# Performance work log

Measured on AMD Instinct MI355X. Metric: run time of the kernel, lower is better.

## Reference

```python
import jax, jax.numpy as jnp
import numpy as np

N = 100000      # total nodes
E = 800000      # directed edges
DIN = 256       # input feature dim
H = 128         # hidden dim
EPS = 1e-5      # BatchNorm eps


def setup_inputs() -> dict:
    key = jax.random.key(0)
    ks = jax.random.split(key, 18)
    s = 0.05
    return {
        "x": jax.random.normal(ks[0], (N, DIN), jnp.float32),
        "src": jax.random.randint(ks[1], (E,), 0, N, dtype=jnp.int32),
        "dst": jax.random.randint(ks[2], (E,), 0, N, dtype=jnp.int32),
        "W1": jax.random.normal(ks[3], (DIN, H), jnp.float32) * s,
        "b1": jnp.zeros((H,), jnp.float32),
        "g1": jnp.ones((H,), jnp.float32),
        "be1": jnp.zeros((H,), jnp.float32),
        "W2": jax.random.normal(ks[4], (H, H), jnp.float32) * s,
        "b2": jnp.zeros((H,), jnp.float32),
        "g2": jnp.ones((H,), jnp.float32),
        "be2": jnp.zeros((H,), jnp.float32),
        "W3": jax.random.normal(ks[5], (H, H), jnp.float32) * s,
        "b3": jnp.zeros((H,), jnp.float32),
        "g3": jnp.ones((H,), jnp.float32),
        "be3": jnp.zeros((H,), jnp.float32),
        "Wf": jax.random.normal(ks[6], (H, 1), jnp.float32) * s,
        "bf": jnp.zeros((1,), jnp.float32),
    }


def _gcn_conv(h, W, b, src, dst, dis):
    # GCNConv: project, then sym-normalized aggregation over edges + self-loops
    h = h @ W                                   # [N, out]
    coef = dis[src] * dis[dst]                  # [E] edge norm weights
    agg = jax.ops.segment_sum(h[src] * coef[:, None], dst, num_segments=N)
    agg = agg + h * (dis * dis)[:, None]        # self-loop term (norm = 1/deg)
    return agg + b


def _bn_relu(h, g, be):
    # BatchNorm1d in training mode (batch stats over nodes, biased variance)
    mu = jnp.mean(h, axis=0)
    var = jnp.var(h, axis=0)
    return jax.nn.relu((h - mu) * (g / jnp.sqrt(var + EPS)) + be)


def reference(x, src, dst, W1, b1, g1, be1, W2, b2, g2, be2,
              W3, b3, g3, be3, Wf, bf):
    # degree of (A + I) counted on destination nodes, edge weight 1
    deg = jax.ops.segment_sum(jnp.ones((E,), jnp.float32), dst, num_segments=N) + 1.0
    dis = jax.lax.rsqrt(deg)                    # deg >= 1, safe

    h = _bn_relu(_gcn_conv(x, W1, b1, src, dst, dis), g1, be1)
    h = _bn_relu(_gcn_conv(h, W2, b2, src, dst, dis), g2, be2)
    h = _bn_relu(_gcn_conv(h, W3, b3, src, dst, dis), g3, be3)
    return h @ Wf + bf                          # [N, 1]
```

## Files before the change

### kernel.cpp

```cpp
#include <hip/hip_runtime.h>
#include <hip/hip_bf16.h>

typedef unsigned short ushort_t;
typedef __bf16 bf16x8 __attribute__((ext_vector_type(8)));
typedef unsigned short ushort8 __attribute__((ext_vector_type(8)));
typedef float f32x4 __attribute__((ext_vector_type(4)));

#define HH 128
#define EPS 1e-5f
#define STAT_SLICES 32

__device__ __forceinline__ float bf2f(ushort_t u) {
    unsigned v = ((unsigned)u) << 16;
    return __builtin_bit_cast(float, v);
}
__device__ __forceinline__ ushort_t f2bf(float f) {
    unsigned u = __builtin_bit_cast(unsigned, f);
    unsigned r = (u + 0x7fffu + ((u >> 16) & 1u)) >> 16;
    return (ushort_t)r;
}
__device__ __forceinline__ float cvt(const void* p, int i, int flag) {
    return flag ? bf2f(((const ushort_t*)p)[i]) : ((const float*)p)[i];
}

__global__ void setupK(const void* g1, const void* b1, const void* b2, const void* b3,
                       const void* g2, const void* g3,
                       const void* be1, const void* be2, const void* be3,
                       const void* Wf, const void* bfp,
                       float* __restrict__ cvec, int* __restrict__ flagp) {
    __shared__ int sflag;
    int t = threadIdx.x;
    if (t == 0) {
        int f = (((const ushort_t*)g1)[0] == 0x3F80) ? 1 : 0;
        sflag = f;
        flagp[0] = f;
    }
    __syncthreads();
    int f = sflag;
    cvec[t]         = cvt(b1, t, f);
    cvec[128 + t]   = cvt(b2, t, f);
    cvec[256 + t]   = cvt(b3, t, f);
    cvec[384 + t]   = cvt(g1, t, f);
    cvec[512 + t]   = cvt(g2, t, f);
    cvec[640 + t]   = cvt(g3, t, f);
    cvec[768 + t]   = cvt(be1, t, f);
    cvec[896 + t]   = cvt(be2, t, f);
    cvec[1024 + t]  = cvt(be3, t, f);
    cvec[1152 + t]  = cvt(Wf, t, f);
    if (t == 0) cvec[1280] = cvt(bfp, 0, f);
}

__global__ void histK(const int* __restrict__ dst, int* __restrict__ counts, int E) {
    int e = blockIdx.x * 256 + threadIdx.x;
    if (e < E) atomicAdd(&counts[dst[e]], 1);
}

__global__ void disK(const int* __restrict__ counts, float* __restrict__ dis, int n) {
    int i = blockIdx.x * 256 + threadIdx.x;
    if (i < n) dis[i] = rsqrtf((float)counts[i] + 1.0f);
}

__global__ void scanA(const int* __restrict__ cnt, int* __restrict__ partial, int n) {
    __shared__ int lds[256];
    int tid = threadIdx.x;
    int base = blockIdx.x * 2048 + tid * 8;
    int s = 0;
#pragma unroll
    for (int j = 0; j < 8; ++j) { int idx = base + j; if (idx < n) s += cnt[idx]; }
    lds[tid] = s; __syncthreads();
    for (int off = 128; off; off >>= 1) { if (tid < off) lds[tid] += lds[tid + off]; __syncthreads(); }
    if (tid == 0) partial[blockIdx.x] = lds[0];
}

__global__ void scanB(int* __restrict__ partial, int* __restrict__ rowptr, int nb, int n) {
    if (threadIdx.x == 0) {
        int running = 0;
        for (int i = 0; i < nb; ++i) { int v = partial[i]; partial[i] = running; running += v; }
        rowptr[n] = running;
    }
}

__global__ void scanC(const int* __restrict__ cnt, const int* __restrict__ partial,
                      int* __restrict__ rowptr, int n) {
    __shared__ int lds[256];
    int tid = threadIdx.x;
    int base = blockIdx.x * 2048 + tid * 8;
    int v[8]; int s = 0;
#pragma unroll
    for (int j = 0; j < 8; ++j) { int idx = base + j; v[j] = (idx < n) ? cnt[idx] : 0; s += v[j]; }
    lds[tid] = s; __syncthreads();
    for (int off = 1; off < 256; off <<= 1) {
        int x = (tid >= off) ? lds[tid - off] : 0;
        __syncthreads();
        lds[tid] += x;
        __syncthreads();
    }
    int excl = lds[tid] - s;
    int off0 = partial[blockIdx.x] + excl;
#pragma unroll
    for (int j = 0; j < 8; ++j) {
        int idx = base + j;
        if (idx < n) { rowptr[idx] = off0; off0 += v[j]; }
    }
}

__global__ void scatterK(const int* __restrict__ src, const int* __restrict__ dst,
                         const int* __restrict__ rowptr, int* __restrict__ fill,
                         const float* __restrict__ dis,
                         uint2* __restrict__ erec, int E) {
    int e = blockIdx.x * 256 + threadIdx.x;
    if (e >= E) return;
    int d = dst[e], s = src[e];
    int old = atomicSub(&fill[d], 1);
    int pos = rowptr[d] + old - 1;
    float c = dis[s] * dis[d];
    uint2 r; r.x = (unsigned)s; r.y = __builtin_bit_cast(unsigned, c);
    erec[pos] = r;
}

__global__ void trK(const void* __restrict__ W1, ushort_t* __restrict__ Wt1,
                    const void* __restrict__ W2, ushort_t* __restrict__ Wt2,
                    const void* __restrict__ W3, ushort_t* __restrict__ Wt3,
                    const int* __restrict__ flagp) {
    int idx = blockIdx.x * 256 + threadIdx.x;
    int flag = flagp[0];
    const void* W; ushort_t* Wt; int Kp;
    if (idx < 32768)       { W = W1; Wt = Wt1; Kp = 264; }
    else if (idx < 49152)  { W = W2; Wt = Wt2; Kp = 136; idx -= 32768; }
    else if (idx < 65536)  { W = W3; Wt = Wt3; Kp = 136; idx -= 49152; }
    else return;
    int k = idx >> 7, n = idx & 127;
    ushort_t v = flag ? ((const ushort_t*)W)[idx] : f2bf(((const float*)W)[idx]);
    Wt[n * Kp + k] = v;
}

template <bool BN, bool EXT, int K>
__global__ __launch_bounds__(256) void mmK(const void* __restrict__ Av,
                                           const ushort_t* __restrict__ Wt,
                                           ushort_t* __restrict__ out,
                                           int n,
                                           const float* __restrict__ scale,
                                           const float* __restrict__ shift,
                                           const int* __restrict__ flagp) {
    constexpr int KP  = K + 8;
    constexpr int BKP = 136;
    constexpr int NCH = K / 128;
    constexpr int NST = K / 32;

    __shared__ ushort_t bs[128 * BKP];

    const int tid  = threadIdx.x;
    const int lane = tid & 63;
    const int wave = tid >> 6;
    const int m = lane & 15;
    const int q = lane >> 4;
    const int flag = EXT ? flagp[0] : 1;

    int rowA = blockIdx.x * 64 + wave * 16 + m;
    int rA = rowA < n ? rowA : (n - 1);

    ushort8 a[NST];
    if (EXT && !flag) {
        const float* ap32 = (const float*)Av + (size_t)rA * K + q * 8;
#pragma unroll
        for (int s = 0; s < NST; ++s) {
            float4 f0 = *(const float4*)(ap32 + s * 32);
            float4 f1 = *(const float4*)(ap32 + s * 32 + 4);
            a[s][0] = f2bf(f0.x); a[s][1] = f2bf(f0.y); a[s][2] = f2bf(f0.z); a[s][3] = f2bf(f0.w);
            a[s][4] = f2bf(f1.x); a[s][5] = f2bf(f1.y); a[s][6] = f2bf(f1.z); a[s][7] = f2bf(f1.w);
        }
    } else {
        const ushort_t* ap16 = (const ushort_t*)Av + (size_t)rA * K + q * 8;
#pragma unroll
        for (int s = 0; s < NST; ++s) a[s] = *(const ushort8*)(ap16 + s * 32);
    }
    if (BN) {
#pragma unroll
        for (int s = 0; s < NST; ++s) {
            int kb = s * 32 + q * 8;
#pragma unroll
            for (int j = 0; j < 8; ++j) {
                float f = fmaxf(bf2f(a[s][j]) * scale[kb + j] + shift[kb + j], 0.f);
                a[s][j] = f2bf(f);
            }
        }
    }

    f32x4 acc[8];
#pragma unroll
    for (int t = 0; t < 8; ++t) acc[t] = (f32x4){0.f, 0.f, 0.f, 0.f};

#pragma unroll
    for (int c = 0; c < NCH; ++c) {
#pragma unroll
        for (int r = 0; r < 8; ++r) {
            int idx = tid + r * 256;
            int row = idx >> 4, seg = idx & 15;
            *(uint4*)&bs[row * BKP + seg * 8] =
                *(const uint4*)&Wt[(size_t)row * KP + c * 128 + seg * 8];
        }
        __syncthreads();
#pragma unroll
        for (int s = 0; s < 4; ++s) {
            bf16x8 af = __builtin_bit_cast(bf16x8, a[c * 4 + s]);
#pragma unroll
            for (int t = 0; t < 8; ++t) {
                ushort8 bv = *(const ushort8*)&bs[(t * 16 + m) * BKP + s * 32 + q * 8];
                acc[t] = __builtin_amdgcn_mfma_f32_16x16x32_bf16(
                    af, __builtin_bit_cast(bf16x8, bv), acc[t], 0, 0, 0);
            }
        }
        if (c + 1 < NCH) __syncthreads();
    }

    const int rb = blockIdx.x * 64 + wave * 16 + q * 4;
#pragma unroll
    for (int t = 0; t < 8; ++t) {
#pragma unroll
        for (int r = 0; r < 4; ++r) {
            int rr = rb + r;
            if (rr < n) out[(size_t)rr * HH + t * 16 + m] = f2bf(acc[t][r]);
        }
    }
}

__global__ __launch_bounds__(256) void aggK(const ushort_t* __restrict__ t,
                                            const uint2* __restrict__ erec,
                                            const int* __restrict__ rowptr,
                                            const float* __restrict__ dis,
                                            const float* __restrict__ bias,
                                            ushort_t* __restrict__ g,
                                            float* __restrict__ ssum, float* __restrict__ ssq,
                                            int n) {
    const int lane = threadIdx.x & 63;
    const int wave = threadIdx.x >> 6;
    const int cb = lane * 2;
    const float b0 = bias[cb], b1 = bias[cb + 1];
    float s0 = 0.f, s1 = 0.f, q0 = 0.f, q1 = 0.f;

    for (int node = blockIdx.x * 4 + wave; node < n; node += gridDim.x * 4) {
        float d = dis[node];
        float d2 = d * d;
        unsigned sv = *(const unsigned*)(t + (size_t)node * HH + cb);
        float a0 = bf2f((ushort_t)(sv & 0xffff)) * d2;
        float a1 = bf2f((ushort_t)(sv >> 16)) * d2;

        int beg = rowptr[node], end = rowptr[node + 1];
        for (int eb = beg; eb < end; eb += 64) {
            int rem = end - eb; if (rem > 64) rem = 64;
            uint2 rec = (lane < rem) ? erec[eb + lane] : (uint2){0u, 0u};
            int es = (int)rec.x;
            float ec = __builtin_bit_cast(float, rec.y);
            int rr = (rem + 7) & ~7;
            for (int j = 0; j < rr; j += 8) {
                int   ii[8]; float cc[8]; unsigned ww[8];
#pragma unroll
                for (int k = 0; k < 8; ++k) {
                    ii[k] = __shfl(es, j + k);
                    cc[k] = __shfl(ec, j + k);
                }
#pragma unroll
                for (int k = 0; k < 8; ++k)
                    ww[k] = *(const unsigned*)(t + (size_t)ii[k] * HH + cb);
#pragma unroll
                for (int k = 0; k < 8; ++k) {
                    a0 += bf2f((ushort_t)(ww[k] & 0xffff)) * cc[k];
                    a1 += bf2f((ushort_t)(ww[k] >> 16)) * cc[k];
                }
            }
        }
        a0 += b0; a1 += b1;
        unsigned packed = (unsigned)f2bf(a0) | ((unsigned)f2bf(a1) << 16);
        *(unsigned*)(g + (size_t)node * HH + cb) = packed;
        s0 += a0; s1 += a1; q0 += a0 * a0; q1 += a1 * a1;
    }

    __shared__ float red[4][64][4];
    red[wave][lane][0] = s0; red[wave][lane][1] = s1;
    red[wave][lane][2] = q0; red[wave][lane][3] = q1;
    __syncthreads();
    if (wave == 0) {
        float S0 = 0, S1 = 0, Q0 = 0, Q1 = 0;
#pragma unroll
        for (int w = 0; w < 4; ++w) {
            S0 += red[w][lane][0]; S1 += red[w][lane][1];
            Q0 += red[w][lane][2]; Q1 += red[w][lane][3];
        }
        int slice = (blockIdx.x & (STAT_SLICES - 1)) * HH;
        atomicAdd(&ssum[slice + cb], S0);
        atomicAdd(&ssum[slice + cb + 1], S1);
        atomicAdd(&ssq[slice + cb], Q0);
        atomicAdd(&ssq[slice + cb + 1], Q1);
    }
}

__global__ void finK(const float* __restrict__ ssum, const float* __restrict__ ssq,
                     const float* __restrict__ gam, const float* __restrict__ bet,
                     float* __restrict__ scale, float* __restrict__ shift, int n) {
    int c = threadIdx.x;
    float S = 0.f, Q = 0.f;
    for (int sl = 0; sl < STAT_SLICES; ++sl) { S += ssum[sl * HH + c]; Q += ssq[sl * HH + c]; }
    float invn = 1.0f / (float)n;
    float mu = S * invn;
    float var = Q * invn - mu * mu;
    var = fmaxf(var, 0.f);
    float sc = gam[c] * rsqrtf(var + EPS);
    scale[c] = sc;
    shift[c] = bet[c] - mu * sc;
}

__global__ __launch_bounds__(256) void outK(const ushort_t* __restrict__ g,
                                            const float* __restrict__ scale,
                                            const float* __restrict__ shift,
                                            const float* __restrict__ Wf,
                                            const float* __restrict__ bfp,
                                            void* __restrict__ outv, int n,
                                            const int* __restrict__ flagp) {
    const int lane = threadIdx.x & 63;
    const int wave = threadIdx.x >> 6;
    const int cb = lane * 2;
    const float w0 = Wf[cb], w1 = Wf[cb + 1];
    const float sc0 = scale[cb], sc1 = scale[cb + 1];
    const float sh0 = shift[cb], sh1 = shift[cb + 1];
    const float bb = bfp[0];
    const int flag = flagp[0];

    for (int node = blockIdx.x * 4 + wave; node < n; node += gridDim.x * 4) {
        unsigned v = *(const unsigned*)(g + (size_t)node * HH + cb);
        float h0 = fmaxf(bf2f((ushort_t)(v & 0xffff)) * sc0 + sh0, 0.f);
        float h1 = fmaxf(bf2f((ushort_t)(v >> 16)) * sc1 + sh1, 0.f);
        float x = h0 * w0 + h1 * w1;
#pragma unroll
        for (int off = 32; off; off >>= 1) x += __shfl_down(x, off);
        if (lane == 0) {
            float r = x + bb;
            if (flag) ((ushort_t*)outv)[node] = f2bf(r);
            else      ((float*)outv)[node] = r;
        }
    }
}

extern "C" void kernel_launch(void* const* d_in, const int* in_sizes, int n_in,
                              void* d_out, int out_size, void* d_ws, size_t ws_size,
                              hipStream_t stream) {
    const int DIN = 256;
    const int N = in_sizes[0] / DIN;
    const int E = in_sizes[1];

    const void* x   = d_in[0];
    const int*  src = (const int*)d_in[1];
    const int*  dst = (const int*)d_in[2];
    const void* W1  = d_in[3];
    const void* b1  = d_in[4];
    const void* g1  = d_in[5];
    const void* be1 = d_in[6];
    const void* W2  = d_in[7];
    const void* b2  = d_in[8];
    const void* g2  = d_in[9];
    const void* be2 = d_in[10];
    const void* W3  = d_in[11];
    const void* b3  = d_in[12];
    const void* g3  = d_in[13];
    const void* be3 = d_in[14];
    const void* Wf  = d_in[15];
    const void* bfp = d_in[16];

    char* base = (char*)d_ws;
    size_t off = 0;
    auto carve = [&](size_t bytes) -> void* {
        void* p = base + off;
        off += (bytes + 255) & ~(size_t)255;
        return p;
    };
    int*      counts = (int*)carve((size_t)N * 4);
    float*    stats  = (float*)carve((size_t)3 * 2 * STAT_SLICES * HH * 4);
    size_t    zbytes = off;
    float*    dis    = (float*)carve((size_t)N * 4);
    int*      rowptr = (int*)carve((size_t)(N + 1) * 4);
    int*      partial= (int*)carve(256 * 4);
    uint2*    erec   = (uint2*)carve((size_t)E * 8);
    ushort_t* Wt1    = (ushort_t*)carve((size_t)128 * 264 * 2);
    ushort_t* Wt2    = (ushort_t*)carve((size_t)128 * 136 * 2);
    ushort_t* Wt3    = (ushort_t*)carve((size_t)128 * 136 * 2);
    ushort_t* tbuf   = (ushort_t*)carve((size_t)N * HH * 2);
    ushort_t* gbuf   = (ushort_t*)carve((size_t)N * HH * 2);
    float*    cvec   = (float*)carve((size_t)1281 * 4);
    int*      flagp  = (int*)carve(256);

    float* ssum0 = stats;                         float* ssq0 = ssum0 + STAT_SLICES * HH;
    float* ssum1 = ssq0 + STAT_SLICES * HH;       float* ssq1 = ssum1 + STAT_SLICES * HH;
    float* ssum2 = ssq1 + STAT_SLICES * HH;       float* ssq2 = ssum2 + STAT_SLICES * HH;

    float* scsh = cvec + 1344;
    float* scshbuf = (float*)carve((size_t)3 * 2 * HH * 4);
    float* scale0 = scshbuf;         float* shift0 = scale0 + HH;
    float* scale1 = shift0 + HH;     float* shift1 = scale1 + HH;
    float* scale2 = shift1 + HH;     float* shift2 = scale2 + HH;
    (void)scsh;

    float* c_b1 = cvec;         float* c_b2 = cvec + 128;  float* c_b3 = cvec + 256;
    float* c_g1 = cvec + 384;   float* c_g2 = cvec + 512;  float* c_g3 = cvec + 640;
    float* c_be1 = cvec + 768;  float* c_be2 = cvec + 896; float* c_be3 = cvec + 1024;
    float* c_Wf = cvec + 1152;  float* c_bf = cvec + 1280;

    const int nb = (N + 2047) / 2048;

    hipMemsetAsync(d_ws, 0, zbytes, stream);

    setupK<<<1, 128, 0, stream>>>(g1, b1, b2, b3, g2, g3, be1, be2, be3, Wf, bfp, cvec, flagp);

    histK<<<(E + 255) / 256, 256, 0, stream>>>(dst, counts, E);
    disK<<<(N + 255) / 256, 256, 0, stream>>>(counts, dis, N);
    scanA<<<nb, 256, 0, stream>>>(counts, partial, N);
    scanB<<<1, 64, 0, stream>>>(partial, rowptr, nb, N);
    scanC<<<nb, 256, 0, stream>>>(counts, partial, rowptr, N);
    scatterK<<<(E + 255) / 256, 256, 0, stream>>>(src, dst, rowptr, counts, dis, erec, E);

    trK<<<256, 256, 0, stream>>>(W1, Wt1, W2, Wt2, W3, Wt3, flagp);

    const int mmBlocks = (N + 63) / 64;
    const int aggBlocks = 4096;

    mmK<false, true, 256><<<mmBlocks, 256, 0, stream>>>(x, Wt1, tbuf, N, nullptr, nullptr, flagp);
    aggK<<<aggBlocks, 256, 0, stream>>>(tbuf, erec, rowptr, dis, c_b1, gbuf, ssum0, ssq0, N);
    finK<<<1, 128, 0, stream>>>(ssum0, ssq0, c_g1, c_be1, scale0, shift0, N);
    mmK<true, false, 128><<<mmBlocks, 256, 0, stream>>>(gbuf, Wt2, tbuf, N, scale0, shift0, flagp);
    aggK<<<aggBlocks, 256, 0, stream>>>(tbuf, erec, rowptr, dis, c_b2, gbuf, ssum1, ssq1, N);
    finK<<<1, 128, 0, stream>>>(ssum1, ssq1, c_g2, c_be2, scale1, shift1, N);
    mmK<true, false, 128><<<mmBlocks, 256, 0, stream>>>(gbuf, Wt3, tbuf, N, scale1, shift1, flagp);
    aggK<<<aggBlocks, 256, 0, stream>>>(tbuf, erec, rowptr, dis, c_b3, gbuf, ssum2, ssq2, N);
    finK<<<1, 128, 0, stream>>>(ssum2, ssq2, c_g3, c_be3, scale2, shift2, N);
    outK<<<1024, 256, 0, stream>>>(gbuf, scale2, shift2, c_Wf, c_bf, d_out, N, flagp);
}
```

Before: 474.7 us.

## Merge preprocessing launches and fold BN finalize into consumer kernels

Merges the setup, histogram and weight-transpose launches into one kernel, fuses dis computation with scanA, and runs scanC inside the first matmul launch. The per-layer finK kernels are removed, and each consumer (mmBNK, outK) now reduces the BN statistics itself into shared memory. The MFMA operand order is swapped so each lane stores four contiguous bf16 outputs per row with vector stores. The aggregation grid is halved. The change targets launch overhead and small serial kernels, at the cost of every block redundantly re-reducing the 32 stat slices.

```diff
diff --git a/kernel.cpp b/kernel.cpp
--- a/kernel.cpp
+++ b/kernel.cpp
@@ -4,6 +4,7 @@
 typedef unsigned short ushort_t;
 typedef __bf16 bf16x8 __attribute__((ext_vector_type(8)));
 typedef unsigned short ushort8 __attribute__((ext_vector_type(8)));
+typedef unsigned short ushort4v __attribute__((ext_vector_type(4)));
 typedef float f32x4 __attribute__((ext_vector_type(4)));
 
 #define HH 128
@@ -23,53 +24,61 @@
     return flag ? bf2f(((const ushort_t*)p)[i]) : ((const float*)p)[i];
 }
 
-__global__ void setupK(const void* g1, const void* b1, const void* b2, const void* b3,
-                       const void* g2, const void* g3,
-                       const void* be1, const void* be2, const void* be3,
-                       const void* Wf, const void* bfp,
-                       float* __restrict__ cvec, int* __restrict__ flagp) {
-    __shared__ int sflag;
-    int t = threadIdx.x;
-    if (t == 0) {
-        int f = (((const ushort_t*)g1)[0] == 0x3F80) ? 1 : 0;
-        sflag = f;
-        flagp[0] = f;
-    }
-    __syncthreads();
-    int f = sflag;
-    cvec[t]         = cvt(b1, t, f);
-    cvec[128 + t]   = cvt(b2, t, f);
-    cvec[256 + t]   = cvt(b3, t, f);
-    cvec[384 + t]   = cvt(g1, t, f);
-    cvec[512 + t]   = cvt(g2, t, f);
-    cvec[640 + t]   = cvt(g3, t, f);
-    cvec[768 + t]   = cvt(be1, t, f);
-    cvec[896 + t]   = cvt(be2, t, f);
-    cvec[1024 + t]  = cvt(be3, t, f);
-    cvec[1152 + t]  = cvt(Wf, t, f);
-    if (t == 0) cvec[1280] = cvt(bfp, 0, f);
-}
-
-__global__ void histK(const int* __restrict__ dst, int* __restrict__ counts, int E) {
-    int e = blockIdx.x * 256 + threadIdx.x;
-    if (e < E) atomicAdd(&counts[dst[e]], 1);
-}
-
-__global__ void disK(const int* __restrict__ counts, float* __restrict__ dis, int n) {
-    int i = blockIdx.x * 256 + threadIdx.x;
-    if (i < n) dis[i] = rsqrtf((float)counts[i] + 1.0f);
-}
-
-__global__ void scanA(const int* __restrict__ cnt, int* __restrict__ partial, int n) {
+__global__ void preK(const int* __restrict__ dst, int* __restrict__ counts, int E,
+                     const void* W1, ushort_t* Wt1, const void* W2, ushort_t* Wt2,
+                     const void* W3, ushort_t* Wt3,
+                     const void* g1, const void* b1, const void* b2, const void* b3,
+                     const void* g2, const void* g3, const void* be1, const void* be2,
+                     const void* be3, const void* Wfp, const void* bfp,
+                     float* __restrict__ cvec, int histB) {
+    const int bid = blockIdx.x;
+    const int tid = threadIdx.x;
+    const int flag = (((const ushort_t*)g1)[0] == 0x3F80) ? 1 : 0;
+    if (bid < histB) {
+        int e = bid * 256 + tid;
+        if (e < E) atomicAdd(&counts[dst[e]], 1);
+    } else if (bid < histB + 256) {
+        int idx = (bid - histB) * 256 + tid;
+        const void* W; ushort_t* Wt; int Kp;
+        if (idx < 32768)      { W = W1; Wt = Wt1; Kp = 264; }
+        else if (idx < 49152) { W = W2; Wt = Wt2; Kp = 136; idx -= 32768; }
+        else                  { W = W3; Wt = Wt3; Kp = 136; idx -= 49152; }
+        int k = idx >> 7, nn = idx & 127;
+        Wt[nn * Kp + k] = flag ? ((const ushort_t*)W)[idx] : f2bf(((const float*)W)[idx]);
+    } else {
+        int t = tid;
+        if (t < 128) {
+            cvec[t]        = cvt(b1, t, flag);
+            cvec[128 + t]  = cvt(b2, t, flag);
+            cvec[256 + t]  = cvt(b3, t, flag);
+            cvec[384 + t]  = cvt(g1, t, flag);
+            cvec[512 + t]  = cvt(g2, t, flag);
+            cvec[640 + t]  = cvt(g3, t, flag);
+            cvec[768 + t]  = cvt(be1, t, flag);
+            cvec[896 + t]  = cvt(be2, t, flag);
+            cvec[1024 + t] = cvt(be3, t, flag);
+            cvec[1152 + t] = cvt(Wfp, t, flag);
+            if (t == 0) cvec[1280] = cvt(bfp, 0, flag);
+        }
+    }
+}
+
+__global__ void scanAdisK(const int* __restrict__ cnt, int* __restrict__ partial,
+                          float* __restrict__ dis, int n, int nbScan) {
     __shared__ int lds[256];
-    int tid = threadIdx.x;
-    int base = blockIdx.x * 2048 + tid * 8;
-    int s = 0;
-#pragma unroll
-    for (int j = 0; j < 8; ++j) { int idx = base + j; if (idx < n) s += cnt[idx]; }
-    lds[tid] = s; __syncthreads();
-    for (int off = 128; off; off >>= 1) { if (tid < off) lds[tid] += lds[tid + off]; __syncthreads(); }
-    if (tid == 0) partial[blockIdx.x] = lds[0];
+    const int tid = threadIdx.x;
+    if ((int)blockIdx.x < nbScan) {
+        int base = blockIdx.x * 2048 + tid * 8;
+        int s = 0;
+#pragma unroll
+        for (int j = 0; j < 8; ++j) { int idx = base + j; if (idx < n) s += cnt[idx]; }
+        lds[tid] = s; __syncthreads();
+        for (int off = 128; off; off >>= 1) { if (tid < off) lds[tid] += lds[tid + off]; __syncthreads(); }
+        if (tid == 0) partial[blockIdx.x] = lds[0];
+    } else {
+        int i = (blockIdx.x - nbScan) * 256 + tid;
+        if (i < n) dis[i] = rsqrtf((float)cnt[i] + 1.0f);
+    }
 }
 
 __global__ void scanB(int* __restrict__ partial, int* __restrict__ rowptr, int nb, int n) {
@@ -80,11 +89,11 @@
     }
 }
 
-__global__ void scanC(const int* __restrict__ cnt, const int* __restrict__ partial,
-                      int* __restrict__ rowptr, int n) {
-    __shared__ int lds[256];
-    int tid = threadIdx.x;
-    int base = blockIdx.x * 2048 + tid * 8;
+__device__ __forceinline__ void scanCDev(int* lds, const int* __restrict__ cnt,
+                                         const int* __restrict__ partial,
+                                         int* __restrict__ rowptr, int n, int bid) {
+    const int tid = threadIdx.x;
+    int base = bid * 2048 + tid * 8;
     int v[8]; int s = 0;
 #pragma unroll
     for (int j = 0; j < 8; ++j) { int idx = base + j; v[j] = (idx < n) ? cnt[idx] : 0; s += v[j]; }
@@ -96,7 +105,7 @@
         __syncthreads();
     }
     int excl = lds[tid] - s;
-    int off0 = partial[blockIdx.x] + excl;
+    int off0 = partial[bid] + excl;
 #pragma unroll
     for (int j = 0; j < 8; ++j) {
         int idx = base + j;
@@ -118,45 +127,47 @@
     erec[pos] = r;
 }
 
-__global__ void trK(const void* __restrict__ W1, ushort_t* __restrict__ Wt1,
-                    const void* __restrict__ W2, ushort_t* __restrict__ Wt2,
-                    const void* __restrict__ W3, ushort_t* __restrict__ Wt3,
-                    const int* __restrict__ flagp) {
-    int idx = blockIdx.x * 256 + threadIdx.x;
-    int flag = flagp[0];
-    const void* W; ushort_t* Wt; int Kp;
-    if (idx < 32768)       { W = W1; Wt = Wt1; Kp = 264; }
-    else if (idx < 49152)  { W = W2; Wt = Wt2; Kp = 136; idx -= 32768; }
-    else if (idx < 65536)  { W = W3; Wt = Wt3; Kp = 136; idx -= 49152; }
-    else return;
-    int k = idx >> 7, n = idx & 127;
-    ushort_t v = flag ? ((const ushort_t*)W)[idx] : f2bf(((const float*)W)[idx]);
-    Wt[n * Kp + k] = v;
-}
-
 template <bool BN, bool EXT, int K>
-__global__ __launch_bounds__(256) void mmK(const void* __restrict__ Av,
-                                           const ushort_t* __restrict__ Wt,
-                                           ushort_t* __restrict__ out,
-                                           int n,
-                                           const float* __restrict__ scale,
-                                           const float* __restrict__ shift,
-                                           const int* __restrict__ flagp) {
+__device__ __forceinline__ void mmDev(char* smemRaw, const void* __restrict__ Av,
+                                      const ushort_t* __restrict__ Wt,
+                                      ushort_t* __restrict__ out, int n,
+                                      const float* __restrict__ ssum,
+                                      const float* __restrict__ ssq,
+                                      const float* __restrict__ gam,
+                                      const float* __restrict__ bet,
+                                      const ushort_t* __restrict__ flagRef, int bid) {
     constexpr int KP  = K + 8;
     constexpr int BKP = 136;
     constexpr int NCH = K / 128;
     constexpr int NST = K / 32;
 
-    __shared__ ushort_t bs[128 * BKP];
+    ushort_t* bs = (ushort_t*)smemRaw;
+    float* scw = (float*)(smemRaw + 128 * BKP * 2);
 
     const int tid  = threadIdx.x;
     const int lane = tid & 63;
     const int wave = tid >> 6;
     const int m = lane & 15;
     const int q = lane >> 4;
-    const int flag = EXT ? flagp[0] : 1;
-
-    int rowA = blockIdx.x * 64 + wave * 16 + m;
+
+    if constexpr (BN) {
+        if (tid < 128) {
+            float S = 0.f, Q = 0.f;
+#pragma unroll
+            for (int sl = 0; sl < STAT_SLICES; ++sl) { S += ssum[sl * HH + tid]; Q += ssq[sl * HH + tid]; }
+            float invn = 1.0f / (float)n;
+            float mu = S * invn;
+            float var = fmaxf(Q * invn - mu * mu, 0.f);
+            float sc = gam[tid] * rsqrtf(var + EPS);
+            scw[tid] = sc;
+            scw[128 + tid] = bet[tid] - mu * sc;
+        }
+        __syncthreads();
+    }
+
+    const int flag = EXT ? ((flagRef[0] == 0x3F80) ? 1 : 0) : 1;
+
+    int rowA = bid * 64 + wave * 16 + m;
     int rA = rowA < n ? rowA : (n - 1);
 
     ushort8 a[NST];
@@ -174,13 +185,13 @@
 #pragma unroll
         for (int s = 0; s < NST; ++s) a[s] = *(const ushort8*)(ap16 + s * 32);
     }
-    if (BN) {
+    if constexpr (BN) {
 #pragma unroll
         for (int s = 0; s < NST; ++s) {
             int kb = s * 32 + q * 8;
 #pragma unroll
             for (int j = 0; j < 8; ++j) {
-                float f = fmaxf(bf2f(a[s][j]) * scale[kb + j] + shift[kb + j], 0.f);
+                float f = fmaxf(bf2f(a[s][j]) * scw[kb + j] + scw[128 + kb + j], 0.f);
                 a[s][j] = f2bf(f);
             }
         }
@@ -202,26 +213,55 @@
         __syncthreads();
 #pragma unroll
         for (int s = 0; s < 4; ++s) {
-            bf16x8 af = __builtin_bit_cast(bf16x8, a[c * 4 + s]);
+            bf16x8 nf = __builtin_bit_cast(bf16x8, a[c * 4 + s]);
 #pragma unroll
             for (int t = 0; t < 8; ++t) {
-                ushort8 bv = *(const ushort8*)&bs[(t * 16 + m) * BKP + s * 32 + q * 8];
+                ushort8 wv = *(const ushort8*)&bs[(t * 16 + m) * BKP + s * 32 + q * 8];
                 acc[t] = __builtin_amdgcn_mfma_f32_16x16x32_bf16(
-                    af, __builtin_bit_cast(bf16x8, bv), acc[t], 0, 0, 0);
+                    __builtin_bit_cast(bf16x8, wv), nf, acc[t], 0, 0, 0);
             }
         }
         if (c + 1 < NCH) __syncthreads();
     }
 
-    const int rb = blockIdx.x * 64 + wave * 16 + q * 4;
-#pragma unroll
-    for (int t = 0; t < 8; ++t) {
-#pragma unroll
-        for (int r = 0; r < 4; ++r) {
-            int rr = rb + r;
-            if (rr < n) out[(size_t)rr * HH + t * 16 + m] = f2bf(acc[t][r]);
-        }
-    }
+    const int node_g = bid * 64 + wave * 16 + m;
+    if (node_g < n) {
+        ushort_t* op = out + (size_t)node_g * HH + q * 4;
+#pragma unroll
+        for (int t = 0; t < 8; ++t) {
+            ushort4v pk;
+#pragma unroll
+            for (int r = 0; r < 4; ++r) pk[r] = f2bf(acc[t][r]);
+            *(ushort4v*)(op + t * 16) = pk;
+        }
+    }
+}
+
+__global__ __launch_bounds__(256) void mm1scanCK(const void* __restrict__ x,
+                                                 const ushort_t* __restrict__ Wt1,
+                                                 ushort_t* __restrict__ tbuf, int n,
+                                                 const ushort_t* __restrict__ flagRef,
+                                                 const int* __restrict__ cnt,
+                                                 const int* __restrict__ partial,
+                                                 int* __restrict__ rowptr, int mmB) {
+    __shared__ char smem[35840];
+    if ((int)blockIdx.x < mmB)
+        mmDev<false, true, 256>(smem, x, Wt1, tbuf, n, nullptr, nullptr, nullptr, nullptr,
+                                flagRef, blockIdx.x);
+    else
+        scanCDev((int*)smem, cnt, partial, rowptr, n, blockIdx.x - mmB);
+}
+
+template <int K>
+__global__ __launch_bounds__(256) void mmBNK(const ushort_t* __restrict__ A,
+                                             const ushort_t* __restrict__ Wt,
+                                             ushort_t* __restrict__ out, int n,
+                                             const float* __restrict__ ssum,
+                                             const float* __restrict__ ssq,
+                                             const float* __restrict__ gam,
+                                             const float* __restrict__ bet) {
+    __shared__ char smem[35840];
+    mmDev<true, false, K>(smem, A, Wt, out, n, ssum, ssq, gam, bet, nullptr, blockIdx.x);
 }
 
 __global__ __launch_bounds__(256) void aggK(const ushort_t* __restrict__ t,
@@ -253,7 +293,7 @@
             float ec = __builtin_bit_cast(float, rec.y);
             int rr = (rem + 7) & ~7;
             for (int j = 0; j < rr; j += 8) {
-                int   ii[8]; float cc[8]; unsigned ww[8];
+                int ii[8]; float cc[8]; unsigned ww[8];
 #pragma unroll
                 for (int k = 0; k < 8; ++k) {
                     ii[k] = __shfl(es, j + k);
@@ -294,36 +334,38 @@
     }
 }
 
-__global__ void finK(const float* __restrict__ ssum, const float* __restrict__ ssq,
-                     const float* __restrict__ gam, const float* __restrict__ bet,
-                     float* __restrict__ scale, float* __restrict__ shift, int n) {
-    int c = threadIdx.x;
-    float S = 0.f, Q = 0.f;
-    for (int sl = 0; sl < STAT_SLICES; ++sl) { S += ssum[sl * HH + c]; Q += ssq[sl * HH + c]; }
-    float invn = 1.0f / (float)n;
-    float mu = S * invn;
-    float var = Q * invn - mu * mu;
-    var = fmaxf(var, 0.f);
-    float sc = gam[c] * rsqrtf(var + EPS);
-    scale[c] = sc;
-    shift[c] = bet[c] - mu * sc;
-}
-
 __global__ __launch_bounds__(256) void outK(const ushort_t* __restrict__ g,
-                                            const float* __restrict__ scale,
-                                            const float* __restrict__ shift,
+                                            const float* __restrict__ ssum,
+                                            const float* __restrict__ ssq,
+                                            const float* __restrict__ gam,
+                                            const float* __restrict__ bet,
                                             const float* __restrict__ Wf,
                                             const float* __restrict__ bfp,
                                             void* __restrict__ outv, int n,
-                                            const int* __restrict__ flagp) {
-    const int lane = threadIdx.x & 63;
-    const int wave = threadIdx.x >> 6;
+                                            const ushort_t* __restrict__ flagRef) {
+    __shared__ float scw[256];
+    const int tid = threadIdx.x;
+    if (tid < 128) {
+        float S = 0.f, Q = 0.f;
+#pragma unroll
+        for (int sl = 0; sl < STAT_SLICES; ++sl) { S += ssum[sl * HH + tid]; Q += ssq[sl * HH + tid]; }
+        float invn = 1.0f / (float)n;
+        float mu = S * invn;
+        float var = fmaxf(Q * invn - mu * mu, 0.f);
+        float sc = gam[tid] * rsqrtf(var + EPS);
+        scw[tid] = sc;
+        scw[128 + tid] = bet[tid] - mu * sc;
+    }
+    __syncthreads();
+
+    const int lane = tid & 63;
+    const int wave = tid >> 6;
     const int cb = lane * 2;
     const float w0 = Wf[cb], w1 = Wf[cb + 1];
-    const float sc0 = scale[cb], sc1 = scale[cb + 1];
-    const float sh0 = shift[cb], sh1 = shift[cb + 1];
+    const float sc0 = scw[cb], sc1 = scw[cb + 1];
+    const float sh0 = scw[128 + cb], sh1 = scw[128 + cb + 1];
     const float bb = bfp[0];
-    const int flag = flagp[0];
+    const int flag = (flagRef[0] == 0x3F80) ? 1 : 0;
 
     for (int node = blockIdx.x * 4 + wave; node < n; node += gridDim.x * 4) {
         unsigned v = *(const unsigned*)(g + (size_t)node * HH + cb);
@@ -364,6 +406,7 @@
     const void* be3 = d_in[14];
     const void* Wf  = d_in[15];
     const void* bfp = d_in[16];
+    const ushort_t* flagRef = (const ushort_t*)g1;
 
     char* base = (char*)d_ws;
     size_t off = 0;
@@ -385,50 +428,37 @@
     ushort_t* tbuf   = (ushort_t*)carve((size_t)N * HH * 2);
     ushort_t* gbuf   = (ushort_t*)carve((size_t)N * HH * 2);
     float*    cvec   = (float*)carve((size_t)1281 * 4);
-    int*      flagp  = (int*)carve(256);
 
     float* ssum0 = stats;                         float* ssq0 = ssum0 + STAT_SLICES * HH;
     float* ssum1 = ssq0 + STAT_SLICES * HH;       float* ssq1 = ssum1 + STAT_SLICES * HH;
     float* ssum2 = ssq1 + STAT_SLICES * HH;       float* ssq2 = ssum2 + STAT_SLICES * HH;
-
-    float* scsh = cvec + 1344;
-    float* scshbuf = (float*)carve((size_t)3 * 2 * HH * 4);
-    float* scale0 = scshbuf;         float* shift0 = scale0 + HH;
-    float* scale1 = shift0 + HH;     float* shift1 = scale1 + HH;
-    float* scale2 = shift1 + HH;     float* shift2 = scale2 + HH;
-    (void)scsh;
 
     float* c_b1 = cvec;         float* c_b2 = cvec + 128;  float* c_b3 = cvec + 256;
     float* c_g1 = cvec + 384;   float* c_g2 = cvec + 512;  float* c_g3 = cvec + 640;
     float* c_be1 = cvec + 768;  float* c_be2 = cvec + 896; float* c_be3 = cvec + 1024;
     float* c_Wf = cvec + 1152;  float* c_bf = cvec + 1280;
 
-    const int nb = (N + 2047) / 2048;
+    const int nbScan = (N + 2047) / 2048;
+    const int histB  = (E + 255) / 256;
+    const int disB   = (N + 255) / 256;
+    const int mmB    = (N + 63) / 64;
+    const int aggB   = 2048;
 
     hipMemsetAsync(d_ws, 0, zbytes, stream);
 
-    setupK<<<1, 128, 0, stream>>>(g1, b1, b2, b3, g2, g3, be1, be2, be3, Wf, bfp, cvec, flagp);
-
-    histK<<<(E + 255) / 256, 256, 0, stream>>>(dst, counts, E);
-    disK<<<(N + 255) / 256, 256, 0, stream>>>(counts, dis, N);
-    scanA<<<nb, 256, 0, stream>>>(counts, partial, N);
-    scanB<<<1, 64, 0, stream>>>(partial, rowptr, nb, N);
-    scanC<<<nb, 256, 0, stream>>>(counts, partial, rowptr, N);
-    scatterK<<<(E + 255) / 256, 256, 0, stream>>>(src, dst, rowptr, counts, dis, erec, E);
-
-    trK<<<256, 256, 0, stream>>>(W1, Wt1, W2, Wt2, W3, Wt3, flagp);
-
-    const int mmBlocks = (N + 63) / 64;
-    const int aggBlocks = 4096;
-
-    mmK<false, true, 256><<<mmBlocks, 256, 0, stream>>>(x, Wt1, tbuf, N, nullptr, nullptr, flagp);
-    aggK<<<aggBlocks, 256, 0, stream>>>(tbuf, erec, rowptr, dis, c_b1, gbuf, ssum0, ssq0, N);
-    finK<<<1, 128, 0, stream>>>(ssum0, ssq0, c_g1, c_be1, scale0, shift0, N);
-    mmK<true, false, 128><<<mmBlocks, 256, 0, stream>>>(gbuf, Wt2, tbuf, N, scale0, shift0, flagp);
-    aggK<<<aggBlocks, 256, 0, stream>>>(tbuf, erec, rowptr, dis, c_b2, gbuf, ssum1, ssq1, N);
-    finK<<<1, 128, 0, stream>>>(ssum1, ssq1, c_g2, c_be2, scale1, shift1, N);
-    mmK<true, false, 128><<<mmBlocks, 256, 0, stream>>>(gbuf, Wt3, tbuf, N, scale1, shift1, flagp);
-    aggK<<<aggBlocks, 256, 0, stream>>>(tbuf, erec, rowptr, dis, c_b3, gbuf, ssum2, ssq2, N);
-    finK<<<1, 128, 0, stream>>>(ssum2, ssq2, c_g3, c_be3, scale2, shift2, N);
-    outK<<<1024, 256, 0, stream>>>(gbuf, scale2, shift2, c_Wf, c_bf, d_out, N, flagp);
-}
+    preK<<<histB + 256 + 1, 256, 0, stream>>>(dst, counts, E, W1, Wt1, W2, Wt2, W3, Wt3,
+                                              g1, b1, b2, b3, g2, g3, be1, be2, be3, Wf, bfp,
+                                              cvec, histB);
+    scanAdisK<<<nbScan + disB, 256, 0, stream>>>(counts, partial, dis, N, nbScan);
+    scanB<<<1, 64, 0, stream>>>(partial, rowptr, nbScan, N);
+    mm1scanCK<<<mmB + nbScan, 256, 0, stream>>>(x, Wt1, tbuf, N, flagRef,
+                                                counts, partial, rowptr, mmB);
+    scatterK<<<histB, 256, 0, stream>>>(src, dst, rowptr, counts, dis, erec, E);
+
+    aggK<<<aggB, 256, 0, stream>>>(tbuf, erec, rowptr, dis, c_b1, gbuf, ssum0, ssq0, N);
+    mmBNK<128><<<mmB, 256, 0, stream>>>(gbuf, Wt2, tbuf, N, ssum0, ssq0, c_g1, c_be1);
+    aggK<<<aggB, 256, 0, stream>>>(tbuf, erec, rowptr, dis, c_b2, gbuf, ssum1, ssq1, N);
+    mmBNK<128><<<mmB, 256, 0, stream>>>(gbuf, Wt3, tbuf, N, ssum1, ssq1, c_g2, c_be2);
+    aggK<<<aggB, 256, 0, stream>>>(tbuf, erec, rowptr, dis, c_b3, gbuf, ssum2, ssq2, N);
+    outK<<<1024, 256, 0, stream>>>(gbuf, ssum2, ssq2, c_g3, c_be3, c_Wf, c_bf, d_out, N, flagRef);
+}
```

New measurement: 459.5 us. 3.2% less time.
